# Optimization experiments

Measured on AMD Instinct MI355X. Metric: run time of the kernel, lower is better.

## Reference

```python
import jax, jax.numpy as jnp
import numpy as np

# Standard MediaPipe FaceMesh lips landmark indices (40 points), as in the source repo.
LIPS_IDX = np.array([
    61, 185, 40, 39, 37, 0, 267, 269, 270, 409,
    291, 146, 91, 181, 84, 17, 314, 405, 321, 375,
    78, 191, 80, 81, 82, 13, 312, 311, 310, 415,
    95, 88, 178, 87, 14, 317, 402, 318, 324, 308,
], dtype=np.int32)

NORMALIZED_LENGTH = 64  # init arg
N_LM = 2 * 21 + 40      # 82 gathered landmarks


def setup_inputs() -> dict:
    key = jax.random.key(0)
    frames = jax.random.normal(key, (32768, 543, 3), dtype=jnp.float32)
    return {"frames": frames}


def reference(frames):
    L = NORMALIZED_LENGTH
    xy = frames[:, :, :2]                      # [T, 543, 2]
    lh = xy[:, 468:489]                        # [T, 21, 2]
    rh = xy[:, 522:543]                        # [T, 21, 2]
    lips = xy[:, LIPS_IDX]                     # [T, 40, 2]
    raw = jnp.concatenate([lh, rh, lips], axis=1)  # [T, 82, 2]
    T = raw.shape[0]

    # Segment boundaries: linspace(0, T-1, L+1) cast to int; segment i = [b[i], b[i+1])
    boundaries = jnp.linspace(0.0, float(T - 1), L + 1).astype(jnp.int32)
    t = jnp.arange(T, dtype=jnp.int32)
    # seg[t] = largest i with boundaries[i] <= t; t >= b[L] maps to L (dropped)
    seg = jnp.searchsorted(boundaries, t, side='right').astype(jnp.int32) - 1

    valid = ~jnp.isnan(raw)
    vf = valid.astype(raw.dtype)
    x0 = jnp.where(valid, raw, jnp.zeros_like(raw))

    cnt = jax.ops.segment_sum(vf, seg, num_segments=L + 1)[:L]   # [L, 82, 2]
    s1 = jax.ops.segment_sum(x0, seg, num_segments=L + 1)[:L]    # [L, 82, 2]
    mean = s1 / cnt                                              # nan if empty segment

    # nan-std: sqrt of nan-mean of squared deviations (two-pass, faithful)
    mean_full = jnp.concatenate([mean, jnp.zeros((1, N_LM, 2), mean.dtype)], axis=0)
    dev = jnp.where(valid, raw - mean_full[seg], jnp.zeros_like(raw))
    s2 = jax.ops.segment_sum(dev * dev, seg, num_segments=L + 1)[:L]
    std = jnp.sqrt(s2 / cnt)

    stats = jnp.concatenate([mean, std], axis=1)                 # [L, 164, 2]
    feats = jnp.where(jnp.isnan(stats), jnp.zeros_like(stats), stats)
    return feats.reshape(L, 2 * 2 * N_LM)                        # [L, 328]
```

## Files before the change

### kernel.cpp

```cpp
#include <hip/hip_runtime.h>
#include <hip/hip_bf16.h>

#define N_SEG 64
#define N_P   164
#define NSP   (N_SEG * N_P)
#define ROW   1629
#define NC    32
#define NC_AT 16

__device__ __constant__ int LIPS[40] = {
    61, 185, 40, 39, 37, 0, 267, 269, 270, 409, 291, 146, 91, 181, 84, 17,
    314, 405, 321, 375, 78, 191, 80, 81, 82, 13, 312, 311, 310, 415, 95, 88,
    178, 87, 14, 317, 402, 318, 324, 308};

__device__ __forceinline__ int landmark_offset(int tid) {
    const int l = tid >> 1;
    const int c = tid & 1;
    int lm;
    if (l < 21)      lm = 468 + l;
    else if (l < 42) lm = 501 + l;
    else             lm = LIPS[l - 42];
    return lm * 3 + c;
}

__device__ __forceinline__ void seg_bounds(int s, int T, int* lo, int* hi) {
    const float step = (float)(T - 1) / 64.0f;
    *lo = (int)((float)s * step);
    *hi = (int)((float)(s + 1) * step);
}

__global__ __launch_bounds__(192) void accum_part(
    const float* __restrict__ frames, float* __restrict__ ws, int T) {
    const int s   = blockIdx.x;
    const int kc  = blockIdx.y;
    const int tid = threadIdx.x;
    if (tid >= N_P) return;

    const int off = landmark_offset(tid);
    int lo, hi;
    seg_bounds(s, T, &lo, &hi);

    float sum = 0.f, sq = 0.f, cnt = 0.f;
    int f = lo + kc;
    for (; f + 7 * NC < hi; f += 8 * NC) {
        float v[8];
#pragma unroll
        for (int u = 0; u < 8; ++u)
            v[u] = frames[(size_t)(f + u * NC) * ROW + off];
#pragma unroll
        for (int u = 0; u < 8; ++u)
            if (v[u] == v[u]) { sum += v[u]; sq = fmaf(v[u], v[u], sq); cnt += 1.f; }
    }
    for (; f < hi; f += NC) {
        float v = frames[(size_t)f * ROW + off];
        if (v == v) { sum += v; sq = fmaf(v, v, sq); cnt += 1.f; }
    }

    const int col = s * N_P + tid;
    ws[(0 * NC + kc) * NSP + col] = sum;
    ws[(1 * NC + kc) * NSP + col] = sq;
    ws[(2 * NC + kc) * NSP + col] = cnt;
}

__global__ __launch_bounds__(192) void finalize_part(
    const float* __restrict__ ws, float* __restrict__ out) {
    const int s = blockIdx.x;
    const int p = threadIdx.x;
    if (p >= N_P) return;

    const int col = s * N_P + p;
    float s1 = 0.f, s2 = 0.f, c = 0.f;
#pragma unroll 8
    for (int kc = 0; kc < NC; ++kc) {
        s1 += ws[(0 * NC + kc) * NSP + col];
        s2 += ws[(1 * NC + kc) * NSP + col];
        c  += ws[(2 * NC + kc) * NSP + col];
    }

    float mean = s1 / c;
    float var  = fmaxf(s2 / c - mean * mean, 0.f);
    float sd   = sqrtf(var);
    if (!(mean == mean)) mean = 0.f;
    if (!(sd == sd))     sd   = 0.f;

    out[s * 328 + p]       = mean;
    out[s * 328 + 164 + p] = sd;
}

__global__ __launch_bounds__(192) void accum_atomic(
    const float* __restrict__ frames, float* __restrict__ ws, int T) {
    const int s   = blockIdx.x;
    const int kc  = blockIdx.y;
    const int tid = threadIdx.x;
    if (tid >= N_P) return;

    const int off = landmark_offset(tid);
    int lo, hi;
    seg_bounds(s, T, &lo, &hi);

    float sum = 0.f, sq = 0.f, cnt = 0.f;
    for (int f = lo + kc; f < hi; f += NC_AT) {
        float v = frames[(size_t)f * ROW + off];
        if (v == v) { sum += v; sq = fmaf(v, v, sq); cnt += 1.f; }
    }

    const int idx = s * N_P + tid;
    atomicAdd(&ws[idx],           sum);
    atomicAdd(&ws[NSP + idx],     sq);
    atomicAdd(&ws[2 * NSP + idx], cnt);
}

__global__ __launch_bounds__(256) void finalize_atomic(
    const float* __restrict__ ws, float* __restrict__ out) {
    const int i = blockIdx.x * blockDim.x + threadIdx.x;
    if (i >= NSP) return;
    const int s = i / N_P;
    const int p = i % N_P;

    const float s1 = ws[i];
    const float s2 = ws[NSP + i];
    const float c  = ws[2 * NSP + i];

    float mean = s1 / c;
    float var  = fmaxf(s2 / c - mean * mean, 0.f);
    float sd   = sqrtf(var);
    if (!(mean == mean)) mean = 0.f;
    if (!(sd == sd))     sd   = 0.f;

    out[s * 328 + p]       = mean;
    out[s * 328 + 164 + p] = sd;
}

extern "C" void kernel_launch(void* const* d_in, const int* in_sizes, int n_in,
                              void* d_out, int out_size, void* d_ws, size_t ws_size,
                              hipStream_t stream) {
    const float* frames = (const float*)d_in[0];
    float* out = (float*)d_out;
    float* ws  = (float*)d_ws;
    const int T = in_sizes[0] / ROW;

    const size_t need = (size_t)3 * NC * NSP * sizeof(float);

    if (ws_size >= need) {
        dim3 grid(N_SEG, NC);
        accum_part<<<grid, 192, 0, stream>>>(frames, ws, T);
        finalize_part<<<N_SEG, 192, 0, stream>>>(ws, out);
    } else {
        hipMemsetAsync(ws, 0, 3 * NSP * sizeof(float), stream);
        dim3 grid(N_SEG, NC_AT);
        accum_atomic<<<grid, 192, 0, stream>>>(frames, ws, T);
        finalize_atomic<<<(NSP + 255) / 256, 256, 0, stream>>>(ws, out);
    }
}
```

Measured before the change: 25.15 us.

## Widen accumulation split and parallelize partial reduction across thread groups

Raises the per-segment chunk split from 32 to 40 blocks and adds a 4-way unrolled middle loop for leftover frames. The finalize kernel now assigns 32 columns per block and splits the 40 partials across 8 groups, combining them through shared memory. This gives more blocks and more memory parallelism to both the gather and the reduction. The cost is a larger workspace, a shared-memory barrier in finalize, and a finalize grid that relies on NSP dividing evenly by 32.

```diff
diff --git a/kernel.cpp b/kernel.cpp
--- a/kernel.cpp
+++ b/kernel.cpp
@@ -5,8 +5,12 @@
 #define N_P   164
 #define NSP   (N_SEG * N_P)
 #define ROW   1629
-#define NC    32
+#define NC    40
 #define NC_AT 16
+
+#define FIN_COLS   32
+#define FIN_GROUPS 8
+#define KC_PER_G   (NC / FIN_GROUPS)
 
 __device__ __constant__ int LIPS[40] = {
     61, 185, 40, 39, 37, 0, 267, 269, 270, 409, 291, 146, 91, 181, 84, 17,
@@ -51,6 +55,15 @@
         for (int u = 0; u < 8; ++u)
             if (v[u] == v[u]) { sum += v[u]; sq = fmaf(v[u], v[u], sq); cnt += 1.f; }
     }
+    for (; f + 3 * NC < hi; f += 4 * NC) {
+        float v[4];
+#pragma unroll
+        for (int u = 0; u < 4; ++u)
+            v[u] = frames[(size_t)(f + u * NC) * ROW + off];
+#pragma unroll
+        for (int u = 0; u < 4; ++u)
+            if (v[u] == v[u]) { sum += v[u]; sq = fmaf(v[u], v[u], sq); cnt += 1.f; }
+    }
     for (; f < hi; f += NC) {
         float v = frames[(size_t)f * ROW + off];
         if (v == v) { sum += v; sq = fmaf(v, v, sq); cnt += 1.f; }
@@ -62,29 +75,46 @@
     ws[(2 * NC + kc) * NSP + col] = cnt;
 }
 
-__global__ __launch_bounds__(192) void finalize_part(
+__global__ __launch_bounds__(256) void finalize_part(
     const float* __restrict__ ws, float* __restrict__ out) {
-    const int s = blockIdx.x;
-    const int p = threadIdx.x;
-    if (p >= N_P) return;
+    const int lane_col = threadIdx.x & (FIN_COLS - 1);
+    const int g        = threadIdx.x >> 5;
+    const int col      = blockIdx.x * FIN_COLS + lane_col;
 
-    const int col = s * N_P + p;
     float s1 = 0.f, s2 = 0.f, c = 0.f;
-#pragma unroll 8
-    for (int kc = 0; kc < NC; ++kc) {
-        s1 += ws[(0 * NC + kc) * NSP + col];
-        s2 += ws[(1 * NC + kc) * NSP + col];
-        c  += ws[(2 * NC + kc) * NSP + col];
+#pragma unroll
+    for (int k = g * KC_PER_G; k < (g + 1) * KC_PER_G; ++k) {
+        s1 += ws[(0 * NC + k) * NSP + col];
+        s2 += ws[(1 * NC + k) * NSP + col];
+        c  += ws[(2 * NC + k) * NSP + col];
     }
 
-    float mean = s1 / c;
-    float var  = fmaxf(s2 / c - mean * mean, 0.f);
-    float sd   = sqrtf(var);
-    if (!(mean == mean)) mean = 0.f;
-    if (!(sd == sd))     sd   = 0.f;
+    __shared__ float ls1[FIN_GROUPS][FIN_COLS];
+    __shared__ float ls2[FIN_GROUPS][FIN_COLS];
+    __shared__ float lc [FIN_GROUPS][FIN_COLS];
+    ls1[g][lane_col] = s1;
+    ls2[g][lane_col] = s2;
+    lc [g][lane_col] = c;
+    __syncthreads();
 
-    out[s * 328 + p]       = mean;
-    out[s * 328 + 164 + p] = sd;
+    if (g == 0) {
+#pragma unroll
+        for (int gg = 1; gg < FIN_GROUPS; ++gg) {
+            s1 += ls1[gg][lane_col];
+            s2 += ls2[gg][lane_col];
+            c  += lc [gg][lane_col];
+        }
+        float mean = s1 / c;
+        float var  = fmaxf(s2 / c - mean * mean, 0.f);
+        float sd   = sqrtf(var);
+        if (!(mean == mean)) mean = 0.f;
+        if (!(sd == sd))     sd   = 0.f;
+
+        const int s = col / N_P;
+        const int p = col % N_P;
+        out[s * 328 + p]       = mean;
+        out[s * 328 + 164 + p] = sd;
+    }
 }
 
 __global__ __launch_bounds__(192) void accum_atomic(
@@ -144,7 +174,7 @@
     if (ws_size >= need) {
         dim3 grid(N_SEG, NC);
         accum_part<<<grid, 192, 0, stream>>>(frames, ws, T);
-        finalize_part<<<N_SEG, 192, 0, stream>>>(ws, out);
+        finalize_part<<<NSP / FIN_COLS, 256, 0, stream>>>(ws, out);
     } else {
         hipMemsetAsync(ws, 0, 3 * NSP * sizeof(float), stream);
         dim3 grid(N_SEG, NC_AT);
```

New measurement: 23.26 us. 1.08x faster.
